# Kernel optimization log

Hardware: AMD Instinct MI355X
Metric: run time of the kernel (lower is better)

The kernel has to match this reference:

```python
import jax, jax.numpy as jnp
import numpy as np

EPS = 1e-5
N, M, ORIG, NBR, F, H, N0 = 100000, 12, 92, 41, 64, 128, 2000


def _bn(x, gamma, beta):
    # BatchNorm1d in training mode: biased batch stats over axis 0
    mu = jnp.mean(x, axis=0)
    var = jnp.var(x, axis=0)
    return (x - mu) * jax.lax.rsqrt(var + EPS) * gamma + beta


def _conv_layer(a, nbr, idx, W, b, g1, bt1, g2, bt2):
    n, m = idx.shape
    f = a.shape[1]
    a_nbr = a[idx]  # (N, M, F) gather
    tot = jnp.concatenate(
        [jnp.broadcast_to(a[:, None, :], (n, m, f)), a_nbr, nbr], axis=2
    )  # (N, M, 2F + nbr_fea_len)
    gated = (tot @ W + b).reshape(n * m, 2 * f)
    gated = _bn(gated, g1, bt1).reshape(n, m, 2 * f)
    filt, core = jnp.split(gated, 2, axis=2)
    summed = jnp.sum(jax.nn.sigmoid(filt) * jax.nn.softplus(core), axis=1)  # (N, F)
    summed = _bn(summed, g2, bt2)
    return jax.nn.softplus(a + summed)


def setup_inputs() -> dict:
    key = jax.random.key(0)
    ks = jax.random.split(key, 24)
    s = lambda shape, k, scale=0.05: jax.random.normal(k, shape, jnp.float32) * scale
    inp = {
        "atom_fea": jax.random.normal(ks[0], (N, ORIG), jnp.float32),
        "nbr_fea": jax.random.normal(ks[1], (N, M, NBR), jnp.float32),
        "nbr_fea_idx": jax.random.randint(ks[2], (N, M), 0, N),
        "crystal_id": jnp.sort(jax.random.randint(ks[3], (N,), 0, N0)),
        # embedding
        "W_emb": s((ORIG, F), ks[4]), "b_emb": s((F,), ks[5]),
        # conv layer
        "cW": s((2 * F + NBR, 2 * F), ks[6]), "cb": s((2 * F,), ks[7]),
        "cg1": jnp.ones((2 * F,), jnp.float32), "cbt1": jnp.zeros((2 * F,), jnp.float32),
        "cg2": jnp.ones((F,), jnp.float32), "cbt2": jnp.zeros((F,), jnp.float32),
        # residual block conv layer
        "rW": s((2 * F + NBR, 2 * F), ks[8]), "rb": s((2 * F,), ks[9]),
        "rg1": jnp.ones((2 * F,), jnp.float32), "rbt1": jnp.zeros((2 * F,), jnp.float32),
        "rg2": jnp.ones((F,), jnp.float32), "rbt2": jnp.zeros((F,), jnp.float32),
        # head
        "W_fc": s((F, H), ks[10]), "b_fc": s((H,), ks[11]),
        "W_out": s((H, 1), ks[12]), "b_out": s((1,), ks[13]),
    }
    return inp


def reference(atom_fea, nbr_fea, nbr_fea_idx, crystal_id,
              W_emb, b_emb, cW, cb, cg1, cbt1, cg2, cbt2,
              rW, rb, rg1, rbt1, rg2, rbt2, W_fc, b_fc, W_out, b_out):
    a = atom_fea @ W_emb + b_emb  # (N, F)
    a1 = _conv_layer(a, nbr_fea, nbr_fea_idx, cW, cb, cg1, cbt1, cg2, cbt2)
    # Res_block: softplus(conv(a1) + a1)
    a2 = jax.nn.softplus(
        _conv_layer(a1, nbr_fea, nbr_fea_idx, rW, rb, rg1, rbt1, rg2, rbt2) + a1
    )
    # per-crystal mean pooling (segment mean)
    cnt = jax.ops.segment_sum(jnp.ones((a2.shape[0],), a2.dtype), crystal_id, N0)
    crys = jax.ops.segment_sum(a2, crystal_id, N0) / jnp.maximum(cnt, 1.0)[:, None]
    crys = jax.nn.softplus(jax.nn.softplus(crys) @ W_fc + b_fc)
    return crys @ W_out + b_out  # (N0, 1)
```

## Files before the change

kernel.cpp:

```cpp
#include <hip/hip_runtime.h>
#include <hip/hip_bf16.h>

namespace {

constexpr int N    = 100000;
constexpr int M    = 12;
constexpr int ORIG = 92;
constexpr int NBR  = 41;
constexpr int F    = 64;
constexpr int H    = 128;
constexpr int N0   = 2000;
constexpr float EPS = 1e-5f;

constexpr int NBLK2 = N / 32;

typedef __attribute__((ext_vector_type(8))) short bf16x8;
typedef __attribute__((ext_vector_type(4))) float f32x4;
typedef float f32x4u __attribute__((ext_vector_type(4), aligned(4)));

__device__ __forceinline__ float u2f(unsigned u){ float f; __builtin_memcpy(&f, &u, 4); return f; }

__device__ __forceinline__ float softplusf(float x){
  float t = __expf(-fabsf(x));
  return fmaxf(x, 0.f) + 0.693147180559945f * __log2f(1.f + t);
}
__device__ __forceinline__ float sigmoidf(float x){
  return __fdividef(1.f, 1.f + __expf(-x));
}
__device__ __forceinline__ unsigned short f2bf(float f){
  __hip_bfloat16 h = __float2bfloat16(f);
  unsigned short u; __builtin_memcpy(&u, &h, 2); return u;
}
__device__ __forceinline__ unsigned packbf2(float lo, float hi){
  __hip_bfloat162 b2 = __float22bfloat162_rn(make_float2(lo, hi));
  unsigned u; __builtin_memcpy(&u, &b2, 4); return u;
}
__device__ __forceinline__ void cvt2(bf16x8& d, int e, float a, float b){
  unsigned u = packbf2(a, b);
  d[e]   = (short)(u & 0xffffu);
  d[e+1] = (short)(u >> 16);
}

__global__ void k_embed(const float* __restrict__ af, const float* __restrict__ W,
                        const float* __restrict__ b, float* __restrict__ a){
  __shared__ float row[4][ORIG];
  int base = blockIdx.x * 4;
  for(int t = threadIdx.x; t < 4*ORIG; t += 256){
    row[t/ORIG][t%ORIG] = af[(size_t)(base + t/ORIG)*ORIG + (t%ORIG)];
  }
  __syncthreads();
  int i = base + (threadIdx.x >> 6);
  int j = threadIdx.x & 63;
  const float* r = row[threadIdx.x >> 6];
  float acc = b[j];
  #pragma unroll
  for(int k = 0; k < ORIG; k++) acc = fmaf(r[k], W[k*F + j], acc);
  a[(size_t)i*F + j] = acc;
}

__global__ void k_prep(const float* __restrict__ W,
                       unsigned short* __restrict__ webf,
                       unsigned short* __restrict__ wspf){
  int b = blockIdx.x;
  int l = threadIdx.x, lr = l & 15, lg = l >> 4;
  if(b < 16){
    int ct = b >> 1, s = b & 1;
    unsigned short* dst = webf + ((size_t)b*64 + l)*8;
    #pragma unroll
    for(int e = 0; e < 8; ++e){
      int k = s*32 + lg*8 + e;
      float w = (k < NBR) ? W[(size_t)(128 + k)*128 + ct*16 + lr] : 0.f;
      dst[e] = f2bf(w);
    }
  } else {
    int f = b - 16;
    int ct = f >> 1, ks = f & 1;
    int col = ct*16 + lr;
    unsigned short* dst = wspf + ((size_t)f*64 + l)*8;
    #pragma unroll
    for(int e = 0; e < 8; ++e){
      int k = ks*32 + lg*8 + e;
      float w = (col < 128) ? W[(size_t)k*128 + col]
                            : W[(size_t)(64 + k)*128 + (col - 128)];
      dst[e] = f2bf(w);
    }
  }
}

__global__ __launch_bounds__(256, 3)
void k_spmm(const float* __restrict__ X, const unsigned short* __restrict__ wspf,
            const float* __restrict__ bias,
            float* __restrict__ S, unsigned* __restrict__ P2u){
  const int tid = threadIdx.x;
  const int l = tid & 63, lr = l & 15, lg = l >> 4;
  const int w = tid >> 6;
  const int a0 = blockIdx.x * 32;
  const bf16x8* wv = (const bf16x8*)wspf;

  bf16x8 BS[2][2], BPl[2], BPh[2];
  #pragma unroll
  for(int c = 0; c < 2; ++c)
    #pragma unroll
    for(int ks = 0; ks < 2; ++ks)
      BS[c][ks] = wv[((2*w + c)*2 + ks)*64 + l];
  #pragma unroll
  for(int ks = 0; ks < 2; ++ks){
    BPl[ks] = wv[((8 + w)*2 + ks)*64 + l];
    BPh[ks] = wv[((12 + w)*2 + ks)*64 + l];
  }

  bf16x8 A[2][2];
  #pragma unroll
  for(int t = 0; t < 2; ++t){
    const float* xr = X + (size_t)(a0 + t*16 + lr)*64;
    #pragma unroll
    for(int ks = 0; ks < 2; ++ks){
      f32x4u v0 = *(const f32x4u*)(xr + ks*32 + lg*8);
      f32x4u v1 = *(const f32x4u*)(xr + ks*32 + lg*8 + 4);
      cvt2(A[t][ks], 0, v0.x, v0.y); cvt2(A[t][ks], 2, v0.z, v0.w);
      cvt2(A[t][ks], 4, v1.x, v1.y); cvt2(A[t][ks], 6, v1.z, v1.w);
    }
  }

  f32x4 DS[2][2], DPl[2], DPh[2];
  #pragma unroll
  for(int t = 0; t < 2; ++t){
    #pragma unroll
    for(int c = 0; c < 2; ++c){
      f32x4 z = {0.f,0.f,0.f,0.f};
      z = __builtin_amdgcn_mfma_f32_16x16x32_bf16(A[t][0], BS[c][0], z, 0, 0, 0);
      z = __builtin_amdgcn_mfma_f32_16x16x32_bf16(A[t][1], BS[c][1], z, 0, 0, 0);
      DS[t][c] = z;
    }
    f32x4 zl = {0.f,0.f,0.f,0.f}, zh = {0.f,0.f,0.f,0.f};
    zl = __builtin_amdgcn_mfma_f32_16x16x32_bf16(A[t][0], BPl[0], zl, 0, 0, 0);
    zl = __builtin_amdgcn_mfma_f32_16x16x32_bf16(A[t][1], BPl[1], zl, 0, 0, 0);
    zh = __builtin_amdgcn_mfma_f32_16x16x32_bf16(A[t][0], BPh[0], zh, 0, 0, 0);
    zh = __builtin_amdgcn_mfma_f32_16x16x32_bf16(A[t][1], BPh[1], zh, 0, 0, 0);
    DPl[t] = zl; DPh[t] = zh;
  }

  float bS[2];
  #pragma unroll
  for(int c = 0; c < 2; ++c) bS[c] = bias[(2*w + c)*16 + lr];

  #pragma unroll
  for(int t = 0; t < 2; ++t){
    #pragma unroll
    for(int r = 0; r < 4; ++r){
      size_t row = a0 + t*16 + lg*4 + r;
      #pragma unroll
      for(int c = 0; c < 2; ++c)
        S[row*128 + (2*w + c)*16 + lr] = DS[t][c][r] + bS[c];
      P2u[row*64 + w*16 + lr] = packbf2(DPl[t][r], DPh[t][r]);
    }
  }
}

template<int MODE>
__global__ __launch_bounds__(256, 3)
void k_pass2(const float* __restrict__ S, const unsigned* __restrict__ P2u,
             const float* __restrict__ nbr, const int* __restrict__ idx,
             const unsigned short* __restrict__ webf,
             const float* __restrict__ sc1, const float* __restrict__ sh1,
             float* __restrict__ SUMb, float* __restrict__ part){
  const int tid = threadIdx.x;
  const int l = tid & 63, lr = l & 15, lg = l >> 4;
  const int wid = tid >> 6, tw = wid >> 1, h = wid & 1;
  const int a0 = blockIdx.x*32 + tw*16;

  bf16x8 Bf[4][2];
  const bf16x8* wv = (const bf16x8*)webf;
  #pragma unroll
  for(int c = 0; c < 4; ++c){
    int cg = (c < 2) ? (2*h + c) : (4 + 2*h + (c - 2));
    Bf[c][0] = wv[(cg*2 + 0)*64 + l];
    Bf[c][1] = wv[(cg*2 + 1)*64 + l];
  }

  float SD[4][4];
  #pragma unroll
  for(int c = 0; c < 4; ++c){
    int col = (c < 2) ? (h*32 + c*16 + lr) : (64 + h*32 + (c - 2)*16 + lr);
    #pragma unroll
    for(int r = 0; r < 4; ++r)
      SD[c][r] = S[(size_t)(a0 + lg*4 + r)*128 + col];
  }

  __shared__ int six[32*M];
  for(int u = tid; u < 32*M; u += 256) six[u] = idx[(size_t)blockIdx.x*32*M + u];
  __syncthreads();

  float c1f[2], h1f[2], c1c[2], h1c[2];
  if(MODE == 1){
    #pragma unroll
    for(int fc = 0; fc < 2; ++fc){
      int j = h*32 + fc*16 + lr;
      c1f[fc] = sc1[j];      h1f[fc] = sh1[j];
      c1c[fc] = sc1[64 + j]; h1c[fc] = sh1[64 + j];
    }
  }

  float sg[4] = {0,0,0,0}, ssg[4] = {0,0,0,0};
  float sact[4][2];
  #pragma unroll
  for(int r = 0; r < 4; ++r){ sact[r][0] = 0.f; sact[r][1] = 0.f; }

  for(int m = 0; m < M; ++m){
    const float* nrow = nbr + ((size_t)(a0 + lr)*M + m)*NBR;
    bf16x8 A0v, A1v = {0,0,0,0,0,0,0,0};
    {
      f32x4u v0 = *(const f32x4u*)(nrow + lg*8);
      f32x4u v1 = *(const f32x4u*)(nrow + lg*8 + 4);
      cvt2(A0v, 0, v0.x, v0.y); cvt2(A0v, 2, v0.z, v0.w);
      cvt2(A0v, 4, v1.x, v1.y); cvt2(A0v, 6, v1.z, v1.w);
    }
    if(lg == 0){
      f32x4u v0 = *(const f32x4u*)(nrow + 32);
      f32x4u v1 = *(const f32x4u*)(nrow + 36);
      cvt2(A1v, 0, v0.x, v0.y); cvt2(A1v, 2, v0.z, v0.w);
      cvt2(A1v, 4, v1.x, v1.y); cvt2(A1v, 6, v1.z, v1.w);
    } else if(lg == 1){
      A1v[0] = (short)f2bf(nrow[40]);
    }

    f32x4 D[4];
    #pragma unroll
    for(int c = 0; c < 4; ++c){
      f32x4 z = {0.f,0.f,0.f,0.f};
      z = __builtin_amdgcn_mfma_f32_16x16x32_bf16(A0v, Bf[c][0], z, 0, 0, 0);
      z = __builtin_amdgcn_mfma_f32_16x16x32_bf16(A1v, Bf[c][1], z, 0, 0, 0);
      D[c] = z;
    }

    #pragma unroll
    for(int r = 0; r < 4; ++r){
      int p = six[(tw*16 + lg*4 + r)*M + m];
      const unsigned* Prow = P2u + (size_t)p*64 + h*32 + lr;
      #pragma unroll
      for(int fc = 0; fc < 2; ++fc){
        unsigned pv = Prow[fc*16];
        float gf = D[fc][r]     + SD[fc][r]     + u2f(pv << 16);
        float gc = D[2 + fc][r] + SD[2 + fc][r] + u2f(pv & 0xffff0000u);
        if(MODE == 0){
          sg[fc]     += gf;  ssg[fc]     = fmaf(gf, gf, ssg[fc]);
          sg[2 + fc] += gc;  ssg[2 + fc] = fmaf(gc, gc, ssg[2 + fc]);
        } else {
          float bf_ = fmaf(gf, c1f[fc], h1f[fc]);
          float bc_ = fmaf(gc, c1c[fc], h1c[fc]);
          sact[r][fc] += sigmoidf(bf_) * softplusf(bc_);
        }
      }
    }
  }

  if(MODE == 0){
    #pragma unroll
    for(int c = 0; c < 4; ++c){
      sg[c]  += __shfl_xor(sg[c], 16, 64);  sg[c]  += __shfl_xor(sg[c], 32, 64);
      ssg[c] += __shfl_xor(ssg[c], 16, 64); ssg[c] += __shfl_xor(ssg[c], 32, 64);
    }
    if(lg == 0){
      float* pb = part + ((size_t)blockIdx.x*2 + tw)*256;
      #pragma unroll
      for(int c = 0; c < 4; ++c){
        int col = (c < 2) ? (h*32 + c*16 + lr) : (64 + h*32 + (c - 2)*16 + lr);
        pb[col]       = sg[c];
        pb[128 + col] = ssg[c];
      }
    }
  } else {
    float ps[2] = {0,0}, pss[2] = {0,0};
    #pragma unroll
    for(int fc = 0; fc < 2; ++fc){
      #pragma unroll
      for(int r = 0; r < 4; ++r){
        float v = sact[r][fc];
        SUMb[(size_t)(a0 + lg*4 + r)*64 + h*32 + fc*16 + lr] = v;
        ps[fc] += v; pss[fc] = fmaf(v, v, pss[fc]);
      }
      ps[fc]  += __shfl_xor(ps[fc], 16, 64);  ps[fc]  += __shfl_xor(ps[fc], 32, 64);
      pss[fc] += __shfl_xor(pss[fc], 16, 64); pss[fc] += __shfl_xor(pss[fc], 32, 64);
    }
    if(lg == 0){
      float* pb = part + ((size_t)blockIdx.x*2 + tw)*128;
      #pragma unroll
      for(int fc = 0; fc < 2; ++fc){
        int j = h*32 + fc*16 + lr;
        pb[j]      = ps[fc];
        pb[64 + j] = pss[fc];
      }
    }
  }
}

__global__ void k_reduce(const float* __restrict__ part, int nblocks, int width,
                         float* __restrict__ out){
  int col = blockIdx.x;
  float s = 0.f;
  for(int b = threadIdx.x; b < nblocks; b += 256) s += part[(size_t)b*width + col];
  __shared__ float red[256];
  red[threadIdx.x] = s;
  __syncthreads();
  for(int off = 128; off; off >>= 1){
    if(threadIdx.x < off) red[threadIdx.x] += red[threadIdx.x + off];
    __syncthreads();
  }
  if(threadIdx.x == 0) out[col] = red[0];
}

__global__ void k_finalize(const float* __restrict__ red, const float* __restrict__ gamma,
                           const float* __restrict__ beta, float* __restrict__ sc,
                           float* __restrict__ sh, float inv, int nch){
  int j = threadIdx.x;
  if(j < nch){
    float mu  = red[j] * inv;
    float var = fmaxf(red[nch + j] * inv - mu*mu, 0.f);
    float r   = rsqrtf(var + EPS);
    float s   = gamma[j] * r;
    sc[j] = s;
    sh[j] = beta[j] - mu * s;
  }
}

__global__ void k_epi(const float* __restrict__ X, const float* __restrict__ SUMb,
                      const float* __restrict__ sc2, const float* __restrict__ sh2,
                      float* __restrict__ Y, int res){
  int stride = gridDim.x * blockDim.x;
  for(int e = blockIdx.x * blockDim.x + threadIdx.x; e < N*F; e += stride){
    int j = e & 63;
    float x = X[e];
    float t = softplusf(x + fmaf(SUMb[e], sc2[j], sh2[j]));
    Y[e] = res ? softplusf(t + x) : t;
  }
}

__global__ void k_pool(const float* __restrict__ A2, const int* __restrict__ cid,
                       float* __restrict__ POOL){
  int c = blockIdx.x;
  int j = threadIdx.x;
  int lo = 0, hi = N;
  while(lo < hi){ int mid = (lo + hi) >> 1; if(cid[mid] < c) lo = mid + 1; else hi = mid; }
  int s0 = lo;
  lo = s0; hi = N;
  while(lo < hi){ int mid = (lo + hi) >> 1; if(cid[mid] < c + 1) lo = mid + 1; else hi = mid; }
  int s1 = lo;
  float s = 0.f;
  for(int i = s0; i < s1; i++) s += A2[(size_t)i*F + j];
  POOL[c*F + j] = s / fmaxf((float)(s1 - s0), 1.f);
}

__global__ void k_head(const float* __restrict__ POOL, const float* __restrict__ Wfc,
                       const float* __restrict__ bfc, const float* __restrict__ Wout,
                       const float* __restrict__ bout, float* __restrict__ out){
  int c = blockIdx.x;
  int t = threadIdx.x;
  __shared__ float spv[F];
  if(t < F) spv[t] = softplusf(POOL[c*F + t]);
  __syncthreads();
  float h = bfc[t];
  #pragma unroll
  for(int k = 0; k < F; k++) h = fmaf(spv[k], Wfc[k*H + t], h);
  h = softplusf(h);
  float v = h * Wout[t];
  #pragma unroll
  for(int off = 32; off; off >>= 1) v += __shfl_down(v, off, 64);
  __shared__ float red[2];
  if((t & 63) == 0) red[t >> 6] = v;
  __syncthreads();
  if(t == 0) out[c] = red[0] + red[1] + bout[0];
}

}

extern "C" void kernel_launch(void* const* d_in, const int* in_sizes, int n_in,
                              void* d_out, int out_size, void* d_ws, size_t ws_size,
                              hipStream_t stream){
  const float* atom_fea = (const float*)d_in[0];
  const float* nbr_fea  = (const float*)d_in[1];
  const int*   nbr_idx  = (const int*)d_in[2];
  const int*   cid      = (const int*)d_in[3];
  const float* W_emb = (const float*)d_in[4];
  const float* b_emb = (const float*)d_in[5];
  const float* cW  = (const float*)d_in[6];
  const float* cb  = (const float*)d_in[7];
  const float* cg1 = (const float*)d_in[8];
  const float* cbt1= (const float*)d_in[9];
  const float* cg2 = (const float*)d_in[10];
  const float* cbt2= (const float*)d_in[11];
  const float* rW  = (const float*)d_in[12];
  const float* rb  = (const float*)d_in[13];
  const float* rg1 = (const float*)d_in[14];
  const float* rbt1= (const float*)d_in[15];
  const float* rg2 = (const float*)d_in[16];
  const float* rbt2= (const float*)d_in[17];
  const float* W_fc = (const float*)d_in[18];
  const float* b_fc = (const float*)d_in[19];
  const float* W_out= (const float*)d_in[20];
  const float* b_out= (const float*)d_in[21];
  float* out = (float*)d_out;

  char* ws = (char*)d_ws;
  float*   A0   = (float*)(ws + 0);
  float*   A1   = (float*)(ws + 25600000);
  float*   SUMb = (float*)(ws + 51200000);
  float*   S    = (float*)(ws + 76800000);
  unsigned* P2u = (unsigned*)(ws + 128000000);
  float*   POOL = (float*)(ws + 153600000);
  float*   SP1  = (float*)(ws + 154200000);
  float*   SP2  = (float*)(ws + 160600000);
  float*   STAT = (float*)(ws + 163800000);
  unsigned short* WEBf = (unsigned short*)(ws + 163900000);
  unsigned short* WSPf = (unsigned short*)(ws + 163932000);
  float* RED1 = STAT;
  float* RED2 = STAT + 256;
  float* SC1  = STAT + 384;
  float* SH1  = STAT + 512;
  float* SC2  = STAT + 640;
  float* SH2  = STAT + 704;

  k_embed<<<N/4, 256, 0, stream>>>(atom_fea, W_emb, b_emb, A0);

  for(int layer = 0; layer < 2; layer++){
    const float* W   = layer ? rW   : cW;
    const float* bb  = layer ? rb   : cb;
    const float* g1  = layer ? rg1  : cg1;
    const float* bt1 = layer ? rbt1 : cbt1;
    const float* g2  = layer ? rg2  : cg2;
    const float* bt2 = layer ? rbt2 : cbt2;
    const float* X = layer ? A1 : A0;
    float*       Y = layer ? A0 : A1;

    k_prep<<<48, 64, 0, stream>>>(W, WEBf, WSPf);
    k_spmm<<<NBLK2, 256, 0, stream>>>(X, WSPf, bb, S, P2u);
    k_pass2<0><<<NBLK2, 256, 0, stream>>>(S, P2u, nbr_fea, nbr_idx,
                                          WEBf, SC1, SH1, nullptr, SP1);
    k_reduce<<<256, 256, 0, stream>>>(SP1, 2*NBLK2, 256, RED1);
    k_finalize<<<1, 128, 0, stream>>>(RED1, g1, bt1, SC1, SH1, 1.f/(float)(N*M), 128);
    k_pass2<1><<<NBLK2, 256, 0, stream>>>(S, P2u, nbr_fea, nbr_idx,
                                          WEBf, SC1, SH1, SUMb, SP2);
    k_reduce<<<128, 256, 0, stream>>>(SP2, 2*NBLK2, 128, RED2);
    k_finalize<<<1, 128, 0, stream>>>(RED2, g2, bt2, SC2, SH2, 1.f/(float)N, 64);
    k_epi<<<2048, 256, 0, stream>>>(X, SUMb, SC2, SH2, Y, layer);
  }

  k_pool<<<N0, 64, 0, stream>>>(A0, cid, POOL);
  k_head<<<N0, 128, 0, stream>>>(POOL, W_fc, b_fc, W_out, b_out, out);
}
```

Baseline: 717.3 us.

## Pre-convert neighbor features to bf16 once and store self-projection as bf16

Adds a one-time kernel that converts the fp32 neighbor feature tensor into a padded bf16 layout (48 per row), so the four pass2 launches read half the bytes with aligned 16-byte loads. The self-projection S is also stored as packed bf16 pairs instead of fp32, halving its write and read traffic. The epilogue is vectorized to float4, and launch bounds are raised to 4 blocks per SM. The trade-off is an extra conversion pass plus workspace, and some precision lost on S. A fallback path is kept for when the workspace is too small.

Result: slower. 1.708 ms (+138.1%).

```diff
diff --git a/kernel.cpp b/kernel.cpp
--- a/kernel.cpp
+++ b/kernel.cpp
@@ -58,6 +58,26 @@
   a[(size_t)i*F + j] = acc;
 }
 
+__global__ void k_nbrcvt(const float* __restrict__ nbr, unsigned short* __restrict__ NB){
+  const long long total = (long long)N*M*6;
+  long long stride = (long long)gridDim.x * blockDim.x;
+  for(long long c = (long long)blockIdx.x*blockDim.x + threadIdx.x; c < total; c += stride){
+    int seg = (int)(c % 6);
+    long long row = c / 6;
+    const float* src = nbr + row*NBR + seg*8;
+    bf16x8 o = {0,0,0,0,0,0,0,0};
+    if(seg < 5){
+      f32x4u v0 = *(const f32x4u*)src;
+      f32x4u v1 = *(const f32x4u*)(src + 4);
+      cvt2(o, 0, v0.x, v0.y); cvt2(o, 2, v0.z, v0.w);
+      cvt2(o, 4, v1.x, v1.y); cvt2(o, 6, v1.z, v1.w);
+    } else {
+      o[0] = (short)f2bf(src[0]);
+    }
+    *(bf16x8*)(NB + c*8) = o;
+  }
+}
+
 __global__ void k_prep(const float* __restrict__ W,
                        unsigned short* __restrict__ webf,
                        unsigned short* __restrict__ wspf){
@@ -87,10 +107,10 @@
   }
 }
 
-__global__ __launch_bounds__(256, 3)
+__global__ __launch_bounds__(256, 4)
 void k_spmm(const float* __restrict__ X, const unsigned short* __restrict__ wspf,
             const float* __restrict__ bias,
-            float* __restrict__ S, unsigned* __restrict__ P2u){
+            unsigned* __restrict__ SU, unsigned* __restrict__ P2u){
   const int tid = threadIdx.x;
   const int l = tid & 63, lr = l & 15, lg = l >> 4;
   const int w = tid >> 6;
@@ -99,14 +119,11 @@
 
   bf16x8 BS[2][2], BPl[2], BPh[2];
   #pragma unroll
-  for(int c = 0; c < 2; ++c)
-    #pragma unroll
-    for(int ks = 0; ks < 2; ++ks)
-      BS[c][ks] = wv[((2*w + c)*2 + ks)*64 + l];
-  #pragma unroll
   for(int ks = 0; ks < 2; ++ks){
-    BPl[ks] = wv[((8 + w)*2 + ks)*64 + l];
-    BPh[ks] = wv[((12 + w)*2 + ks)*64 + l];
+    BS[0][ks] = wv[((w)*2 + ks)*64 + l];
+    BS[1][ks] = wv[((4 + w)*2 + ks)*64 + l];
+    BPl[ks]   = wv[((8 + w)*2 + ks)*64 + l];
+    BPh[ks]   = wv[((12 + w)*2 + ks)*64 + l];
   }
 
   bf16x8 A[2][2];
@@ -140,28 +157,24 @@
     DPl[t] = zl; DPh[t] = zh;
   }
 
-  float bS[2];
-  #pragma unroll
-  for(int c = 0; c < 2; ++c) bS[c] = bias[(2*w + c)*16 + lr];
+  float b0 = bias[w*16 + lr], b1 = bias[64 + w*16 + lr];
 
   #pragma unroll
   for(int t = 0; t < 2; ++t){
     #pragma unroll
     for(int r = 0; r < 4; ++r){
       size_t row = a0 + t*16 + lg*4 + r;
-      #pragma unroll
-      for(int c = 0; c < 2; ++c)
-        S[row*128 + (2*w + c)*16 + lr] = DS[t][c][r] + bS[c];
+      SU[row*64 + w*16 + lr]  = packbf2(DS[t][0][r] + b0, DS[t][1][r] + b1);
       P2u[row*64 + w*16 + lr] = packbf2(DPl[t][r], DPh[t][r]);
     }
   }
 }
 
-template<int MODE>
-__global__ __launch_bounds__(256, 3)
-void k_pass2(const float* __restrict__ S, const unsigned* __restrict__ P2u,
-             const float* __restrict__ nbr, const int* __restrict__ idx,
-             const unsigned short* __restrict__ webf,
+template<int MODE, int NBF>
+__global__ __launch_bounds__(256, 4)
+void k_pass2(const unsigned* __restrict__ SU, const unsigned* __restrict__ P2u,
+             const float* __restrict__ nbr, const unsigned short* __restrict__ NB,
+             const int* __restrict__ idx, const unsigned short* __restrict__ webf,
              const float* __restrict__ sc1, const float* __restrict__ sh1,
              float* __restrict__ SUMb, float* __restrict__ part){
   const int tid = threadIdx.x;
@@ -180,12 +193,13 @@
 
   float SD[4][4];
   #pragma unroll
-  for(int c = 0; c < 4; ++c){
-    int col = (c < 2) ? (h*32 + c*16 + lr) : (64 + h*32 + (c - 2)*16 + lr);
-    #pragma unroll
-    for(int r = 0; r < 4; ++r)
-      SD[c][r] = S[(size_t)(a0 + lg*4 + r)*128 + col];
-  }
+  for(int fc = 0; fc < 2; ++fc)
+    #pragma unroll
+    for(int r = 0; r < 4; ++r){
+      unsigned sv = SU[(size_t)(a0 + lg*4 + r)*64 + h*32 + fc*16 + lr];
+      SD[fc][r]     = u2f(sv << 16);
+      SD[2 + fc][r] = u2f(sv & 0xffff0000u);
+    }
 
   __shared__ int six[32*M];
   for(int u = tid; u < 32*M; u += 256) six[u] = idx[(size_t)blockIdx.x*32*M + u];
@@ -207,21 +221,25 @@
   for(int r = 0; r < 4; ++r){ sact[r][0] = 0.f; sact[r][1] = 0.f; }
 
   for(int m = 0; m < M; ++m){
-    const float* nrow = nbr + ((size_t)(a0 + lr)*M + m)*NBR;
     bf16x8 A0v, A1v = {0,0,0,0,0,0,0,0};
-    {
+    if constexpr(NBF){
+      const unsigned short* nrow = NB + ((size_t)(a0 + lr)*M + m)*48;
+      A0v = *(const bf16x8*)(nrow + lg*8);
+      if(lg < 2) A1v = *(const bf16x8*)(nrow + 32 + lg*8);
+    } else {
+      const float* nrow = nbr + ((size_t)(a0 + lr)*M + m)*NBR;
       f32x4u v0 = *(const f32x4u*)(nrow + lg*8);
       f32x4u v1 = *(const f32x4u*)(nrow + lg*8 + 4);
       cvt2(A0v, 0, v0.x, v0.y); cvt2(A0v, 2, v0.z, v0.w);
       cvt2(A0v, 4, v1.x, v1.y); cvt2(A0v, 6, v1.z, v1.w);
-    }
-    if(lg == 0){
-      f32x4u v0 = *(const f32x4u*)(nrow + 32);
-      f32x4u v1 = *(const f32x4u*)(nrow + 36);
-      cvt2(A1v, 0, v0.x, v0.y); cvt2(A1v, 2, v0.z, v0.w);
-      cvt2(A1v, 4, v1.x, v1.y); cvt2(A1v, 6, v1.z, v1.w);
-    } else if(lg == 1){
-      A1v[0] = (short)f2bf(nrow[40]);
+      if(lg == 0){
+        f32x4u w0 = *(const f32x4u*)(nrow + 32);
+        f32x4u w1 = *(const f32x4u*)(nrow + 36);
+        cvt2(A1v, 0, w0.x, w0.y); cvt2(A1v, 2, w0.z, w0.w);
+        cvt2(A1v, 4, w1.x, w1.y); cvt2(A1v, 6, w1.z, w1.w);
+      } else if(lg == 1){
+        A1v[0] = (short)f2bf(nrow[40]);
+      }
     }
 
     f32x4 D[4];
@@ -327,11 +345,18 @@
                       const float* __restrict__ sc2, const float* __restrict__ sh2,
                       float* __restrict__ Y, int res){
   int stride = gridDim.x * blockDim.x;
-  for(int e = blockIdx.x * blockDim.x + threadIdx.x; e < N*F; e += stride){
-    int j = e & 63;
-    float x = X[e];
-    float t = softplusf(x + fmaf(SUMb[e], sc2[j], sh2[j]));
-    Y[e] = res ? softplusf(t + x) : t;
+  int total = N*F/4;
+  for(int e4 = blockIdx.x * blockDim.x + threadIdx.x; e4 < total; e4 += stride){
+    f32x4 x = *(const f32x4*)(X + (size_t)e4*4);
+    f32x4 s = *(const f32x4*)(SUMb + (size_t)e4*4);
+    int j0 = (e4*4) & 63;
+    f32x4 y;
+    #pragma unroll
+    for(int u = 0; u < 4; ++u){
+      float t = softplusf(x[u] + fmaf(s[u], sc2[j0 + u], sh2[j0 + u]));
+      y[u] = res ? softplusf(t + x[u]) : t;
+    }
+    *(f32x4*)(Y + (size_t)e4*4) = y;
   }
 }
 
@@ -370,6 +395,20 @@
   __syncthreads();
   if(t == 0) out[c] = red[0] + red[1] + bout[0];
 }
+
+constexpr size_t OFF_A0   = 0;
+constexpr size_t OFF_A1   = 25600000;
+constexpr size_t OFF_SUMB = 51200000;
+constexpr size_t OFF_SU   = 76800000;
+constexpr size_t OFF_P2U  = 102400000;
+constexpr size_t OFF_POOL = 128000000;
+constexpr size_t OFF_SP1  = 128512000;
+constexpr size_t OFF_SP2  = 134912000;
+constexpr size_t OFF_STAT = 138112000;
+constexpr size_t OFF_WEBF = 138120192;
+constexpr size_t OFF_WSPF = 138136576;
+constexpr size_t OFF_NB   = 138169344;
+constexpr size_t WS_NEED_NB = OFF_NB + (size_t)N*M*48*2;
 
 }
 
@@ -401,17 +440,18 @@
   float* out = (float*)d_out;
 
   char* ws = (char*)d_ws;
-  float*   A0   = (float*)(ws + 0);
-  float*   A1   = (float*)(ws + 25600000);
-  float*   SUMb = (float*)(ws + 51200000);
-  float*   S    = (float*)(ws + 76800000);
-  unsigned* P2u = (unsigned*)(ws + 128000000);
-  float*   POOL = (float*)(ws + 153600000);
-  float*   SP1  = (float*)(ws + 154200000);
-  float*   SP2  = (float*)(ws + 160600000);
-  float*   STAT = (float*)(ws + 163800000);
-  unsigned short* WEBf = (unsigned short*)(ws + 163900000);
-  unsigned short* WSPf = (unsigned short*)(ws + 163932000);
+  float*    A0   = (float*)(ws + OFF_A0);
+  float*    A1   = (float*)(ws + OFF_A1);
+  float*    SUMb = (float*)(ws + OFF_SUMB);
+  unsigned* SU   = (unsigned*)(ws + OFF_SU);
+  unsigned* P2u  = (unsigned*)(ws + OFF_P2U);
+  float*    POOL = (float*)(ws + OFF_POOL);
+  float*    SP1  = (float*)(ws + OFF_SP1);
+  float*    SP2  = (float*)(ws + OFF_SP2);
+  float*    STAT = (float*)(ws + OFF_STAT);
+  unsigned short* WEBf = (unsigned short*)(ws + OFF_WEBF);
+  unsigned short* WSPf = (unsigned short*)(ws + OFF_WSPF);
+  unsigned short* NB   = (unsigned short*)(ws + OFF_NB);
   float* RED1 = STAT;
   float* RED2 = STAT + 256;
   float* SC1  = STAT + 384;
@@ -419,7 +459,10 @@
   float* SC2  = STAT + 640;
   float* SH2  = STAT + 704;
 
+  const bool use_nb = (ws_size >= WS_NEED_NB);
+
   k_embed<<<N/4, 256, 0, stream>>>(atom_fea, W_emb, b_emb, A0);
+  if(use_nb) k_nbrcvt<<<2048, 256, 0, stream>>>(nbr_fea, NB);
 
   for(int layer = 0; layer < 2; layer++){
     const float* W   = layer ? rW   : cW;
@@ -432,13 +475,23 @@
     float*       Y = layer ? A0 : A1;
 
     k_prep<<<48, 64, 0, stream>>>(W, WEBf, WSPf);
-    k_spmm<<<NBLK2, 256, 0, stream>>>(X, WSPf, bb, S, P2u);
-    k_pass2<0><<<NBLK2, 256, 0, stream>>>(S, P2u, nbr_fea, nbr_idx,
-                                          WEBf, SC1, SH1, nullptr, SP1);
+    k_spmm<<<NBLK2, 256, 0, stream>>>(X, WSPf, bb, SU, P2u);
+    if(use_nb){
+      k_pass2<0,1><<<NBLK2, 256, 0, stream>>>(SU, P2u, nbr_fea, NB, nbr_idx,
+                                              WEBf, SC1, SH1, nullptr, SP1);
+    } else {
+      k_pass2<0,0><<<NBLK2, 256, 0, stream>>>(SU, P2u, nbr_fea, nullptr, nbr_idx,
+                                              WEBf, SC1, SH1, nullptr, SP1);
+    }
     k_reduce<<<256, 256, 0, stream>>>(SP1, 2*NBLK2, 256, RED1);
     k_finalize<<<1, 128, 0, stream>>>(RED1, g1, bt1, SC1, SH1, 1.f/(float)(N*M), 128);
-    k_pass2<1><<<NBLK2, 256, 0, stream>>>(S, P2u, nbr_fea, nbr_idx,
-                                          WEBf, SC1, SH1, SUMb, SP2);
+    if(use_nb){
+      k_pass2<1,1><<<NBLK2, 256, 0, stream>>>(SU, P2u, nbr_fea, NB, nbr_idx,
+                                              WEBf, SC1, SH1, SUMb, SP2);
+    } else {
+      k_pass2<1,0><<<NBLK2, 256, 0, stream>>>(SU, P2u, nbr_fea, nullptr, nbr_idx,
+                                              WEBf, SC1, SH1, SUMb, SP2);
+    }
     k_reduce<<<128, 256, 0, stream>>>(SP2, 2*NBLK2, 128, RED2);
     k_finalize<<<1, 128, 0, stream>>>(RED2, g2, bt2, SC2, SH2, 1.f/(float)N, 64);
     k_epi<<<2048, 256, 0, stream>>>(X, SUMb, SC2, SH2, Y, layer);
```
